# Kernel tuning notes

Hardware: AMD Instinct MI355X
Metric: run time of the kernel (lower is better)

## Reference

```python
import jax, jax.numpy as jnp
import numpy as np
from jax import lax

B, T, IN, H = 32, 512, 512, 512
NUM_LAYERS, NUM_DIR = 2, 2


def _lstm_layer(inputs, Wx, Wh, bx, bh, reverse):
    """inputs: [T,B,D]; Wx: [4H,D]; Wh: [4H,H]; bx,bh: [4H]. Returns (hs [T,B,H], hT, cT)."""
    Tn, Bn, _ = inputs.shape
    Hn = Wh.shape[1]
    # Precompute input-to-hidden projections for all timesteps (one big GEMM).
    xg = jnp.einsum('tbd,gd->tbg', inputs, Wx) + bx + bh  # [T,B,4H]
    if reverse:
        xg = xg[::-1]

    def step(carry, xg_t):
        h, c = carry
        g = xg_t + h @ Wh.T  # [B,4H]
        i, f, gg, o = jnp.split(g, 4, axis=-1)  # PyTorch LSTM gate order i,f,g,o
        i = jax.nn.sigmoid(i)
        f = jax.nn.sigmoid(f)
        gg = jnp.tanh(gg)
        o = jax.nn.sigmoid(o)
        c = f * c + i * gg
        h = o * jnp.tanh(c)
        return (h, c), h

    h0 = jnp.zeros((Bn, Hn), dtype=inputs.dtype)
    (hT, cT), hs = lax.scan(step, (h0, h0), xg)
    if reverse:
        hs = hs[::-1]
    return hs, hT, cT


def setup_inputs() -> dict:
    key = jax.random.key(0)
    ks = jax.random.split(key, 20)
    std = 1.0 / np.sqrt(H)
    u = lambda k, shp: jax.random.uniform(k, shp, jnp.float32, -std, std)
    inp = {
        'x': jax.random.normal(ks[0], (B, T, IN), jnp.float32),
        # layer 0: input dim IN, stacked over 2 directions
        'Wx_l0': u(ks[1], (NUM_DIR, 4 * H, IN)),
        'Wh_l0': u(ks[2], (NUM_DIR, 4 * H, H)),
        'bx_l0': u(ks[3], (NUM_DIR, 4 * H)),
        'bh_l0': u(ks[4], (NUM_DIR, 4 * H)),
        # layer 1: input dim 2H (bidirectional concat)
        'Wx_l1': u(ks[5], (NUM_DIR, 4 * H, NUM_DIR * H)),
        'Wh_l1': u(ks[6], (NUM_DIR, 4 * H, H)),
        'bx_l1': u(ks[7], (NUM_DIR, 4 * H)),
        'bh_l1': u(ks[8], (NUM_DIR, 4 * H)),
    }
    return inp


def reference(x, Wx_l0, Wh_l0, bx_l0, bh_l0, Wx_l1, Wh_l1, bx_l1, bh_l1):
    layer_params = [(Wx_l0, Wh_l0, bx_l0, bh_l0), (Wx_l1, Wh_l1, bx_l1, bh_l1)]
    inputs = jnp.transpose(x, (1, 0, 2))  # [T,B,IN] (batch_first -> time-major)
    h_list, c_list = [], []
    for layer in range(NUM_LAYERS):
        Wx, Wh, bx, bh = layer_params[layer]
        dir_outs = []
        for d in range(NUM_DIR):
            hs, hT, cT = _lstm_layer(inputs, Wx[d], Wh[d], bx[d], bh[d], reverse=(d == 1))
            dir_outs.append(hs)
            h_list.append(hT)
            c_list.append(cT)
        inputs = jnp.concatenate(dir_outs, axis=-1)  # [T,B,2H] (dropout=0.0)
    output = jnp.transpose(inputs, (1, 0, 2))  # [B,T,2H]
    h_n = jnp.stack(h_list)  # [num_layers*num_dir, B, H]
    c_n = jnp.stack(c_list)
    return output, h_n, c_n
```

## Files before the change

kernel.cpp:

```cpp
#include <hip/hip_runtime.h>

typedef _Float16 f16;
typedef _Float16 f16x2 __attribute__((ext_vector_type(2)));
typedef _Float16 f16x4 __attribute__((ext_vector_type(4)));
typedef _Float16 f16x8 __attribute__((ext_vector_type(8)));
typedef float f32x4 __attribute__((ext_vector_type(4)));

#define AS1 __attribute__((address_space(1)))
#define AS3 __attribute__((address_space(3)))

static __device__ __forceinline__ float sigf(float x) { return 1.f / (1.f + __expf(-x)); }
static __device__ __forceinline__ float tanh_f(float x) { return 2.f / (1.f + __expf(-2.f * x)) - 1.f; }

__global__ void f2h_kernel(const float* __restrict__ in, f16* __restrict__ out, int n4) {
  const int i = blockIdx.x * blockDim.x + threadIdx.x;
  if (i >= n4) return;
  const float4 v = ((const float4*)in)[i];
  f16x4 o;
  o[0] = (f16)v.x; o[1] = (f16)v.y; o[2] = (f16)v.z; o[3] = (f16)v.w;
  ((f16x4*)out)[i] = o;
}

__global__ void bias_kernel(const float* __restrict__ a, const float* __restrict__ b,
                            float* __restrict__ o, int n) {
  const int i = blockIdx.x * blockDim.x + threadIdx.x;
  if (i < n) o[i] = a[i] + b[i];
}

__global__ __launch_bounds__(256) void gemm_xg(const f16* __restrict__ A,
                                               const f16* __restrict__ Bt,
                                               const float* __restrict__ bias,
                                               f16* __restrict__ outp, int K) {
  __shared__ f16 As[128 * 64];
  __shared__ f16 Bs[128 * 64];
  const int tid = threadIdx.x;
  const int w = tid >> 6, l = tid & 63;
  const int m0 = blockIdx.x << 7, n0 = blockIdx.y << 7;
  const int wm = w >> 1, wn = w & 1;
  f32x4 acc[4][4] = {};

  const int lr8 = l >> 3, lc8 = l & 7;
  const int gcol = (lc8 ^ lr8) << 3;

  for (int k0 = 0; k0 < K; k0 += 64) {
    __syncthreads();
#pragma unroll
    for (int j = 0; j < 4; ++j) {
      const int i = (w << 2) + j;
      const f16* ga = A + (size_t)(m0 + (i << 3) + lr8) * K + (k0 + gcol);
      __builtin_amdgcn_global_load_lds((const AS1 void*)ga, (AS3 void*)(As + (i << 9)), 16, 0, 0);
      const f16* gb = Bt + (size_t)(n0 + (i << 3) + lr8) * K + (k0 + gcol);
      __builtin_amdgcn_global_load_lds((const AS1 void*)gb, (AS3 void*)(Bs + (i << 9)), 16, 0, 0);
    }
    asm volatile("s_waitcnt vmcnt(0)" ::: "memory");
    __syncthreads();

#pragma unroll
    for (int kk = 0; kk < 2; ++kk) {
      const int cb = (kk << 6) + ((l >> 4) << 4);
      f16x8 af[4], bf[4];
#pragma unroll
      for (int a = 0; a < 4; ++a) {
        const int r = (wm << 6) + (a << 4) + (l & 15);
        af[a] = *(const f16x8*)((const char*)As + r * 128 + (cb ^ ((r & 7) << 4)));
      }
#pragma unroll
      for (int b = 0; b < 4; ++b) {
        const int r = (wn << 6) + (b << 4) + (l & 15);
        bf[b] = *(const f16x8*)((const char*)Bs + r * 128 + (cb ^ ((r & 7) << 4)));
      }
#pragma unroll
      for (int a = 0; a < 4; ++a)
#pragma unroll
        for (int b = 0; b < 4; ++b)
          acc[a][b] = __builtin_amdgcn_mfma_f32_16x16x32_f16(af[a], bf[b], acc[a][b], 0, 0, 0);
    }
  }

#pragma unroll
  for (int b = 0; b < 4; ++b) {
    const int col = n0 + (wn << 6) + (b << 4) + (l & 15);
    const float bv = bias[col];
    f16* ob = outp + (size_t)(col >> 11) * (16384ull * 2048) + (col & 2047);
#pragma unroll
    for (int a = 0; a < 4; ++a) {
      const int row0 = m0 + (wm << 6) + (a << 4) + ((l >> 4) << 2);
#pragma unroll
      for (int r = 0; r < 4; ++r)
        ob[(size_t)(row0 + r) * 2048] = (f16)(acc[a][b][r] + bv);
    }
  }
}

__global__ __launch_bounds__(256) void lstm_scan(const f16* __restrict__ Whb,
                                                 const f16* __restrict__ xg,
                                                 unsigned long long* __restrict__ ring,
                                                 f16* __restrict__ h0_all,
                                                 float* __restrict__ outf,
                                                 float* __restrict__ hn,
                                                 float* __restrict__ cn,
                                                 const int layer) {
  __shared__ f16 Wh_s[64 * 512];
  __shared__ f16 h_s[32 * 512];
  __shared__ float G_s[4 * 32 * 18];

  const int tid = threadIdx.x;
  const int dir = blockIdx.x >> 5;
  const int s = blockIdx.x & 31;
  const int w = tid >> 6, l = tid & 63;

#pragma unroll
  for (int j = 0; j < 16; ++j) {
    const int chunk = (j << 8) + tid;
    const int lr = chunk >> 6;
    const int cbyte = (chunk & 63) << 4;
    const int g = lr >> 4, u = lr & 15;
    const char* src = (const char*)Whb + (((size_t)dir * 2048 + (g << 9) + (s << 4) + u) << 10) + cbyte;
    const uint4 v = *(const uint4*)src;
    *(uint4*)((char*)Wh_s + (lr << 10) + (cbyte ^ ((lr & 7) << 4))) = v;
  }

  unsigned long long* rdir = ring + ((size_t)dir << 15);
  const int bb = tid >> 3;
  const int up = tid & 7;

  float c0 = 0.f, c1 = 0.f;
  __syncthreads();

#pragma unroll 1
  for (int t = 0; t < 512; ++t) {
    const int tau = dir ? (511 - t) : t;
    const f16* xr = xg + (((size_t)dir * 16384 + (size_t)bb * 512 + (size_t)tau) << 11) + (s << 4) + (up << 1);
    const f16x2 xv0 = *(const f16x2*)(xr);
    const f16x2 xv1 = *(const f16x2*)(xr + 512);
    const f16x2 xv2 = *(const f16x2*)(xr + 1024);
    const f16x2 xv3 = *(const f16x2*)(xr + 1536);

    float pi0 = 0.f, pi1 = 0.f, pf0 = 0.f, pf1 = 0.f, pg0 = 0.f, pg1 = 0.f, po0 = 0.f, po1 = 0.f;

    if (t > 0) {
      const unsigned tgt = (unsigned)t;
      const unsigned long long* rs = rdir + ((size_t)(t & 3) << 13);
      unsigned long long v[8][4];
#pragma unroll
      for (int j = 0; j < 8; ++j) {
        const int chunk = (j << 8) + tid;
        const unsigned long long* sp = rs + ((chunk >> 6) << 8) + ((chunk & 63) << 2);
#pragma unroll
        for (int q = 0; q < 4; ++q)
          v[j][q] = __hip_atomic_load(sp + q, __ATOMIC_RELAXED, __HIP_MEMORY_SCOPE_AGENT);
      }
#pragma unroll
      for (int j = 0; j < 8; ++j) {
        const int chunk = (j << 8) + tid;
        const int b = chunk >> 6;
        const unsigned long long* sp = rs + (b << 8) + ((chunk & 63) << 2);
        int guard = 0;
        while (!(((unsigned)v[j][0] == tgt) & ((unsigned)v[j][1] == tgt) &
                 ((unsigned)v[j][2] == tgt) & ((unsigned)v[j][3] == tgt))) {
#pragma unroll
          for (int q = 0; q < 4; ++q)
            v[j][q] = __hip_atomic_load(sp + q, __ATOMIC_RELAXED, __HIP_MEMORY_SCOPE_AGENT);
          if (++guard > (1 << 20)) break;
        }
        uint4 d;
        d.x = (unsigned)(v[j][0] >> 32);
        d.y = (unsigned)(v[j][1] >> 32);
        d.z = (unsigned)(v[j][2] >> 32);
        d.w = (unsigned)(v[j][3] >> 32);
        const int cbyte = (chunk & 63) << 4;
        *(uint4*)((char*)h_s + (b << 10) + (cbyte ^ ((b & 7) << 4))) = d;
      }
      __syncthreads();

      f32x4 acc0 = {}, acc1 = {};
#pragma unroll
      for (int kk = 0; kk < 16; ++kk) {
        const int cb = (kk << 6) + ((l >> 4) << 4);
        const int ra0 = l & 15;
        const int ra1 = 16 + ra0;
        const int rb = (w << 4) + ra0;
        const f16x8 a0 = *(const f16x8*)((const char*)h_s + (ra0 << 10) + (cb ^ ((ra0 & 7) << 4)));
        const f16x8 a1 = *(const f16x8*)((const char*)h_s + (ra1 << 10) + (cb ^ ((ra1 & 7) << 4)));
        const f16x8 bv = *(const f16x8*)((const char*)Wh_s + (rb << 10) + (cb ^ ((rb & 7) << 4)));
        acc0 = __builtin_amdgcn_mfma_f32_16x16x32_f16(a0, bv, acc0, 0, 0, 0);
        acc1 = __builtin_amdgcn_mfma_f32_16x16x32_f16(a1, bv, acc1, 0, 0, 0);
      }
#pragma unroll
      for (int r = 0; r < 4; ++r) {
        const int dr = ((l >> 4) << 2) + r;
        G_s[((w << 5) + dr) * 18 + (l & 15)] = acc0[r];
        G_s[((w << 5) + 16 + dr) * 18 + (l & 15)] = acc1[r];
      }
      __syncthreads();

      const float* gp = G_s + bb * 18 + (up << 1);
      const float2 vi = *(const float2*)(gp);
      const float2 vf = *(const float2*)(gp + 576);
      const float2 vg = *(const float2*)(gp + 1152);
      const float2 vo = *(const float2*)(gp + 1728);
      pi0 = vi.x; pi1 = vi.y; pf0 = vf.x; pf1 = vf.y;
      pg0 = vg.x; pg1 = vg.y; po0 = vo.x; po1 = vo.y;
    }

    pi0 += (float)xv0[0]; pi1 += (float)xv0[1];
    pf0 += (float)xv1[0]; pf1 += (float)xv1[1];
    pg0 += (float)xv2[0]; pg1 += (float)xv2[1];
    po0 += (float)xv3[0]; po1 += (float)xv3[1];

    const float i0 = sigf(pi0), i1 = sigf(pi1);
    const float f0 = sigf(pf0), f1 = sigf(pf1);
    const float g0 = tanh_f(pg0), g1 = tanh_f(pg1);
    const float o0 = sigf(po0), o1 = sigf(po1);
    c0 = f0 * c0 + i0 * g0;
    c1 = f1 * c1 + i1 * g1;
    const float h0v = o0 * tanh_f(c0);
    const float h1v = o1 * tanh_f(c1);

    union { f16x2 h2; unsigned u; } pk;
    pk.h2[0] = (f16)h0v; pk.h2[1] = (f16)h1v;

    {
      const size_t ridx = ((size_t)((t + 1) & 3) << 13) + ((size_t)bb << 8) + (s << 3) + up;
      const unsigned long long pv = ((unsigned long long)pk.u << 32) | (unsigned long long)(t + 1);
      __hip_atomic_store(rdir + ridx, pv, __ATOMIC_RELAXED, __HIP_MEMORY_SCOPE_AGENT);
    }

    const size_t orow = (((size_t)bb * 512 + (size_t)tau) << 10) + ((size_t)dir << 9) + (s << 4) + (up << 1);
    if (layer == 0) {
      *(unsigned*)(h0_all + orow) = pk.u;
    } else {
      *(float2*)(outf + orow) = make_float2(h0v, h1v);
    }
    if (t == 511) {
      const size_t nidx = (((size_t)(layer << 1) + (size_t)dir) << 14) + ((size_t)bb << 9) + (s << 4) + (up << 1);
      *(float2*)(hn + nidx) = make_float2(h0v, h1v);
      *(float2*)(cn + nidx) = make_float2(c0, c1);
    }
  }
}

extern "C" void kernel_launch(void* const* d_in, const int* in_sizes, int n_in,
                              void* d_out, int out_size, void* d_ws, size_t ws_size,
                              hipStream_t stream) {
  const float* x = (const float*)d_in[0];
  const float* Wx0 = (const float*)d_in[1];
  const float* Wh0 = (const float*)d_in[2];
  const float* bx0 = (const float*)d_in[3];
  const float* bh0 = (const float*)d_in[4];
  const float* Wx1 = (const float*)d_in[5];
  const float* Wh1 = (const float*)d_in[6];
  const float* bx1 = (const float*)d_in[7];
  const float* bh1 = (const float*)d_in[8];

  char* ws = (char*)d_ws;
  size_t off = 0;
  auto alloc = [&](size_t b) { char* p = ws + off; off += (b + 255) & ~(size_t)255; return p; };
  f16* xg = (f16*)alloc(2ull * 16384 * 2048 * 2);
  f16* x_h = (f16*)alloc(16384ull * 512 * 2);
  f16* h0a = (f16*)alloc(16384ull * 1024 * 2);
  f16* Wx0h = (f16*)alloc(2ull * 2048 * 512 * 2);
  f16* Wh0h = (f16*)alloc(2ull * 2048 * 512 * 2);
  f16* Wx1h = (f16*)alloc(2ull * 2048 * 1024 * 2);
  f16* Wh1h = (f16*)alloc(2ull * 2048 * 512 * 2);
  float* bias0 = (float*)alloc(4096 * 4);
  float* bias1 = (float*)alloc(4096 * 4);
  unsigned long long* ring0 = (unsigned long long*)alloc(2ull * 4 * 32 * 256 * 8);
  unsigned long long* ring1 = (unsigned long long*)alloc(2ull * 4 * 32 * 256 * 8);
  if (off > ws_size) return;

  float* outp = (float*)d_out;
  float* hn = outp + 16384ull * 1024;
  float* cn = hn + 4ull * 32 * 512;

  hipMemsetAsync(ring0, 0, 2ull * 4 * 32 * 256 * 8, stream);
  hipMemsetAsync(ring1, 0, 2ull * 4 * 32 * 256 * 8, stream);

  f2h_kernel<<<dim3(2097152 / 256), 256, 0, stream>>>(x, x_h, 2097152);
  f2h_kernel<<<dim3(524288 / 256), 256, 0, stream>>>(Wx0, Wx0h, 524288);
  f2h_kernel<<<dim3(524288 / 256), 256, 0, stream>>>(Wh0, Wh0h, 524288);
  f2h_kernel<<<dim3(1048576 / 256), 256, 0, stream>>>(Wx1, Wx1h, 1048576);
  f2h_kernel<<<dim3(524288 / 256), 256, 0, stream>>>(Wh1, Wh1h, 524288);
  bias_kernel<<<16, 256, 0, stream>>>(bx0, bh0, bias0, 4096);
  bias_kernel<<<16, 256, 0, stream>>>(bx1, bh1, bias1, 4096);

  dim3 g(128, 32);
  gemm_xg<<<g, 256, 0, stream>>>(x_h, Wx0h, bias0, xg, 512);
  lstm_scan<<<64, 256, 0, stream>>>(Wh0h, xg, ring0, h0a, nullptr, hn, cn, 0);
  gemm_xg<<<g, 256, 0, stream>>>(h0a, Wx1h, bias1, xg, 1024);
  lstm_scan<<<64, 256, 0, stream>>>(Wh1h, xg, ring1, nullptr, outp, hn, cn, 1);
}
```

Measured before the change: 5.187 ms.

## Add per-block step counters for polling and batch output stores over eight steps

Each block now publishes its completed step in a small per-direction counter array. Waiting blocks first spin on these 32 counters and only then read the h ring once, instead of spinning on every ring entry. The ring tag becomes step XOR payload, so a stale value cannot pass the check. Output h stores are buffered in registers for eight timesteps and written together, which moves global writes off the serial recurrence path. The costs are an extra barrier per step and a counter store that, being relaxed with no fence, could become visible before the ring data, which the retained per-entry check still covers.

```diff
diff --git a/kernel.cpp b/kernel.cpp
--- a/kernel.cpp
+++ b/kernel.cpp
@@ -95,6 +95,7 @@
 __global__ __launch_bounds__(256) void lstm_scan(const f16* __restrict__ Whb,
                                                  const f16* __restrict__ xg,
                                                  unsigned long long* __restrict__ ring,
+                                                 unsigned* __restrict__ sums,
                                                  f16* __restrict__ h0_all,
                                                  float* __restrict__ outf,
                                                  float* __restrict__ hn,
@@ -121,121 +122,150 @@
   }
 
   unsigned long long* rdir = ring + ((size_t)dir << 15);
+  unsigned* sum = sums + (((layer << 1) + dir) << 6);
   const int bb = tid >> 3;
   const int up = tid & 7;
 
   float c0 = 0.f, c1 = 0.f;
   __syncthreads();
 
-#pragma unroll 1
-  for (int t = 0; t < 512; ++t) {
-    const int tau = dir ? (511 - t) : t;
-    const f16* xr = xg + (((size_t)dir * 16384 + (size_t)bb * 512 + (size_t)tau) << 11) + (s << 4) + (up << 1);
-    const f16x2 xv0 = *(const f16x2*)(xr);
-    const f16x2 xv1 = *(const f16x2*)(xr + 512);
-    const f16x2 xv2 = *(const f16x2*)(xr + 1024);
-    const f16x2 xv3 = *(const f16x2*)(xr + 1536);
-
-    float pi0 = 0.f, pi1 = 0.f, pf0 = 0.f, pf1 = 0.f, pg0 = 0.f, pg1 = 0.f, po0 = 0.f, po1 = 0.f;
-
-    if (t > 0) {
-      const unsigned tgt = (unsigned)t;
-      const unsigned long long* rs = rdir + ((size_t)(t & 3) << 13);
-      unsigned long long v[8][4];
-#pragma unroll
-      for (int j = 0; j < 8; ++j) {
-        const int chunk = (j << 8) + tid;
-        const unsigned long long* sp = rs + ((chunk >> 6) << 8) + ((chunk & 63) << 2);
-#pragma unroll
-        for (int q = 0; q < 4; ++q)
-          v[j][q] = __hip_atomic_load(sp + q, __ATOMIC_RELAXED, __HIP_MEMORY_SCOPE_AGENT);
-      }
-#pragma unroll
-      for (int j = 0; j < 8; ++j) {
-        const int chunk = (j << 8) + tid;
-        const int b = chunk >> 6;
-        const unsigned long long* sp = rs + (b << 8) + ((chunk & 63) << 2);
-        int guard = 0;
-        while (!(((unsigned)v[j][0] == tgt) & ((unsigned)v[j][1] == tgt) &
-                 ((unsigned)v[j][2] == tgt) & ((unsigned)v[j][3] == tgt))) {
+  for (int tb = 0; tb < 512; tb += 8) {
+    unsigned svh[8];
+    float2 svo[8];
+#pragma unroll
+    for (int ti = 0; ti < 8; ++ti) {
+      const int t = tb + ti;
+      const int tau = dir ? (511 - t) : t;
+      float pi0 = 0.f, pi1 = 0.f, pf0 = 0.f, pf1 = 0.f, pg0 = 0.f, pg1 = 0.f, po0 = 0.f, po1 = 0.f;
+
+      if (t > 0) {
+        const unsigned tgt = (unsigned)t;
+        {
+          const unsigned* sw = sum + (tid & 31);
+          int guard = 0;
+          unsigned v;
+          do {
+            v = __hip_atomic_load(sw, __ATOMIC_RELAXED, __HIP_MEMORY_SCOPE_AGENT);
+          } while (v < tgt && ++guard < (1 << 20));
+        }
+        __syncthreads();
+
+        const unsigned long long* rs = rdir + ((size_t)(t & 3) << 13);
+        unsigned long long v[8][4];
+#pragma unroll
+        for (int j = 0; j < 8; ++j) {
+          const int chunk = (j << 8) + tid;
+          const unsigned long long* sp = rs + ((chunk >> 6) << 8) + ((chunk & 63) << 2);
 #pragma unroll
           for (int q = 0; q < 4; ++q)
             v[j][q] = __hip_atomic_load(sp + q, __ATOMIC_RELAXED, __HIP_MEMORY_SCOPE_AGENT);
-          if (++guard > (1 << 20)) break;
-        }
-        uint4 d;
-        d.x = (unsigned)(v[j][0] >> 32);
-        d.y = (unsigned)(v[j][1] >> 32);
-        d.z = (unsigned)(v[j][2] >> 32);
-        d.w = (unsigned)(v[j][3] >> 32);
-        const int cbyte = (chunk & 63) << 4;
-        *(uint4*)((char*)h_s + (b << 10) + (cbyte ^ ((b & 7) << 4))) = d;
-      }
-      __syncthreads();
-
-      f32x4 acc0 = {}, acc1 = {};
-#pragma unroll
-      for (int kk = 0; kk < 16; ++kk) {
-        const int cb = (kk << 6) + ((l >> 4) << 4);
-        const int ra0 = l & 15;
-        const int ra1 = 16 + ra0;
-        const int rb = (w << 4) + ra0;
-        const f16x8 a0 = *(const f16x8*)((const char*)h_s + (ra0 << 10) + (cb ^ ((ra0 & 7) << 4)));
-        const f16x8 a1 = *(const f16x8*)((const char*)h_s + (ra1 << 10) + (cb ^ ((ra1 & 7) << 4)));
-        const f16x8 bv = *(const f16x8*)((const char*)Wh_s + (rb << 10) + (cb ^ ((rb & 7) << 4)));
-        acc0 = __builtin_amdgcn_mfma_f32_16x16x32_f16(a0, bv, acc0, 0, 0, 0);
-        acc1 = __builtin_amdgcn_mfma_f32_16x16x32_f16(a1, bv, acc1, 0, 0, 0);
-      }
-#pragma unroll
-      for (int r = 0; r < 4; ++r) {
-        const int dr = ((l >> 4) << 2) + r;
-        G_s[((w << 5) + dr) * 18 + (l & 15)] = acc0[r];
-        G_s[((w << 5) + 16 + dr) * 18 + (l & 15)] = acc1[r];
-      }
-      __syncthreads();
-
-      const float* gp = G_s + bb * 18 + (up << 1);
-      const float2 vi = *(const float2*)(gp);
-      const float2 vf = *(const float2*)(gp + 576);
-      const float2 vg = *(const float2*)(gp + 1152);
-      const float2 vo = *(const float2*)(gp + 1728);
-      pi0 = vi.x; pi1 = vi.y; pf0 = vf.x; pf1 = vf.y;
-      pg0 = vg.x; pg1 = vg.y; po0 = vo.x; po1 = vo.y;
-    }
-
-    pi0 += (float)xv0[0]; pi1 += (float)xv0[1];
-    pf0 += (float)xv1[0]; pf1 += (float)xv1[1];
-    pg0 += (float)xv2[0]; pg1 += (float)xv2[1];
-    po0 += (float)xv3[0]; po1 += (float)xv3[1];
-
-    const float i0 = sigf(pi0), i1 = sigf(pi1);
-    const float f0 = sigf(pf0), f1 = sigf(pf1);
-    const float g0 = tanh_f(pg0), g1 = tanh_f(pg1);
-    const float o0 = sigf(po0), o1 = sigf(po1);
-    c0 = f0 * c0 + i0 * g0;
-    c1 = f1 * c1 + i1 * g1;
-    const float h0v = o0 * tanh_f(c0);
-    const float h1v = o1 * tanh_f(c1);
-
-    union { f16x2 h2; unsigned u; } pk;
-    pk.h2[0] = (f16)h0v; pk.h2[1] = (f16)h1v;
-
-    {
-      const size_t ridx = ((size_t)((t + 1) & 3) << 13) + ((size_t)bb << 8) + (s << 3) + up;
-      const unsigned long long pv = ((unsigned long long)pk.u << 32) | (unsigned long long)(t + 1);
-      __hip_atomic_store(rdir + ridx, pv, __ATOMIC_RELAXED, __HIP_MEMORY_SCOPE_AGENT);
-    }
-
-    const size_t orow = (((size_t)bb * 512 + (size_t)tau) << 10) + ((size_t)dir << 9) + (s << 4) + (up << 1);
-    if (layer == 0) {
-      *(unsigned*)(h0_all + orow) = pk.u;
-    } else {
-      *(float2*)(outf + orow) = make_float2(h0v, h1v);
-    }
-    if (t == 511) {
-      const size_t nidx = (((size_t)(layer << 1) + (size_t)dir) << 14) + ((size_t)bb << 9) + (s << 4) + (up << 1);
-      *(float2*)(hn + nidx) = make_float2(h0v, h1v);
-      *(float2*)(cn + nidx) = make_float2(c0, c1);
+        }
+#pragma unroll
+        for (int j = 0; j < 8; ++j) {
+          const int chunk = (j << 8) + tid;
+          const int b = chunk >> 6;
+          const unsigned long long* sp = rs + (b << 8) + ((chunk & 63) << 2);
+          int guard = 0;
+          while (!((((unsigned)v[j][0] ^ (unsigned)(v[j][0] >> 32)) == tgt) &
+                   (((unsigned)v[j][1] ^ (unsigned)(v[j][1] >> 32)) == tgt) &
+                   (((unsigned)v[j][2] ^ (unsigned)(v[j][2] >> 32)) == tgt) &
+                   (((unsigned)v[j][3] ^ (unsigned)(v[j][3] >> 32)) == tgt))) {
+#pragma unroll
+            for (int q = 0; q < 4; ++q)
+              v[j][q] = __hip_atomic_load(sp + q, __ATOMIC_RELAXED, __HIP_MEMORY_SCOPE_AGENT);
+            if (++guard > (1 << 20)) break;
+          }
+          uint4 d;
+          d.x = (unsigned)(v[j][0] >> 32);
+          d.y = (unsigned)(v[j][1] >> 32);
+          d.z = (unsigned)(v[j][2] >> 32);
+          d.w = (unsigned)(v[j][3] >> 32);
+          const int cbyte = (chunk & 63) << 4;
+          *(uint4*)((char*)h_s + (b << 10) + (cbyte ^ ((b & 7) << 4))) = d;
+        }
+        __syncthreads();
+      }
+
+      const f16* xr = xg + (((size_t)dir * 16384 + (size_t)bb * 512 + (size_t)tau) << 11) + (s << 4) + (up << 1);
+      const f16x2 xv0 = *(const f16x2*)(xr);
+      const f16x2 xv1 = *(const f16x2*)(xr + 512);
+      const f16x2 xv2 = *(const f16x2*)(xr + 1024);
+      const f16x2 xv3 = *(const f16x2*)(xr + 1536);
+
+      if (t > 0) {
+        f32x4 acc0 = {}, acc1 = {};
+#pragma unroll
+        for (int kk = 0; kk < 16; ++kk) {
+          const int cb = (kk << 6) + ((l >> 4) << 4);
+          const int ra0 = l & 15;
+          const int ra1 = 16 + ra0;
+          const int rb = (w << 4) + ra0;
+          const f16x8 a0 = *(const f16x8*)((const char*)h_s + (ra0 << 10) + (cb ^ ((ra0 & 7) << 4)));
+          const f16x8 a1 = *(const f16x8*)((const char*)h_s + (ra1 << 10) + (cb ^ ((ra1 & 7) << 4)));
+          const f16x8 bv = *(const f16x8*)((const char*)Wh_s + (rb << 10) + (cb ^ ((rb & 7) << 4)));
+          acc0 = __builtin_amdgcn_mfma_f32_16x16x32_f16(a0, bv, acc0, 0, 0, 0);
+          acc1 = __builtin_amdgcn_mfma_f32_16x16x32_f16(a1, bv, acc1, 0, 0, 0);
+        }
+#pragma unroll
+        for (int r = 0; r < 4; ++r) {
+          const int dr = ((l >> 4) << 2) + r;
+          G_s[((w << 5) + dr) * 18 + (l & 15)] = acc0[r];
+          G_s[((w << 5) + 16 + dr) * 18 + (l & 15)] = acc1[r];
+        }
+        __syncthreads();
+
+        const float* gp = G_s + bb * 18 + (up << 1);
+        const float2 vi = *(const float2*)(gp);
+        const float2 vf = *(const float2*)(gp + 576);
+        const float2 vg = *(const float2*)(gp + 1152);
+        const float2 vo = *(const float2*)(gp + 1728);
+        pi0 = vi.x; pi1 = vi.y; pf0 = vf.x; pf1 = vf.y;
+        pg0 = vg.x; pg1 = vg.y; po0 = vo.x; po1 = vo.y;
+      }
+
+      pi0 += (float)xv0[0]; pi1 += (float)xv0[1];
+      pf0 += (float)xv1[0]; pf1 += (float)xv1[1];
+      pg0 += (float)xv2[0]; pg1 += (float)xv2[1];
+      po0 += (float)xv3[0]; po1 += (float)xv3[1];
+
+      const float i0 = sigf(pi0), i1 = sigf(pi1);
+      const float f0 = sigf(pf0), f1 = sigf(pf1);
+      const float g0 = tanh_f(pg0), g1 = tanh_f(pg1);
+      const float o0 = sigf(po0), o1 = sigf(po1);
+      c0 = f0 * c0 + i0 * g0;
+      c1 = f1 * c1 + i1 * g1;
+      const float h0v = o0 * tanh_f(c0);
+      const float h1v = o1 * tanh_f(c1);
+
+      union { f16x2 h2; unsigned u; } pk;
+      pk.h2[0] = (f16)h0v; pk.h2[1] = (f16)h1v;
+
+      {
+        const size_t ridx = ((size_t)((t + 1) & 3) << 13) + ((size_t)bb << 8) + (s << 3) + up;
+        const unsigned long long pv =
+            ((unsigned long long)pk.u << 32) | (unsigned long long)((unsigned)(t + 1) ^ pk.u);
+        __hip_atomic_store(rdir + ridx, pv, __ATOMIC_RELAXED, __HIP_MEMORY_SCOPE_AGENT);
+      }
+      if (tid == 0)
+        __hip_atomic_store(sum + s, (unsigned)(t + 1), __ATOMIC_RELAXED, __HIP_MEMORY_SCOPE_AGENT);
+
+      if (layer == 0) svh[ti] = pk.u;
+      else            svo[ti] = make_float2(h0v, h1v);
+
+      if (t == 511) {
+        const size_t nidx = (((size_t)(layer << 1) + (size_t)dir) << 14) + ((size_t)bb << 9) + (s << 4) + (up << 1);
+        *(float2*)(hn + nidx) = make_float2(h0v, h1v);
+        *(float2*)(cn + nidx) = make_float2(c0, c1);
+      }
+    }
+
+#pragma unroll
+    for (int ti = 0; ti < 8; ++ti) {
+      const int t = tb + ti;
+      const int tau = dir ? (511 - t) : t;
+      const size_t orow = (((size_t)bb * 512 + (size_t)tau) << 10) + ((size_t)dir << 9) + (s << 4) + (up << 1);
+      if (layer == 0) *(unsigned*)(h0_all + orow) = svh[ti];
+      else            *(float2*)(outf + orow) = svo[ti];
     }
   }
 }
@@ -267,6 +297,7 @@
   float* bias1 = (float*)alloc(4096 * 4);
   unsigned long long* ring0 = (unsigned long long*)alloc(2ull * 4 * 32 * 256 * 8);
   unsigned long long* ring1 = (unsigned long long*)alloc(2ull * 4 * 32 * 256 * 8);
+  unsigned* sums = (unsigned*)alloc(4ull * 64 * 4);
   if (off > ws_size) return;
 
   float* outp = (float*)d_out;
@@ -275,6 +306,7 @@
 
   hipMemsetAsync(ring0, 0, 2ull * 4 * 32 * 256 * 8, stream);
   hipMemsetAsync(ring1, 0, 2ull * 4 * 32 * 256 * 8, stream);
+  hipMemsetAsync(sums, 0, 4ull * 64 * 4, stream);
 
   f2h_kernel<<<dim3(2097152 / 256), 256, 0, stream>>>(x, x_h, 2097152);
   f2h_kernel<<<dim3(524288 / 256), 256, 0, stream>>>(Wx0, Wx0h, 524288);
@@ -286,7 +318,7 @@
 
   dim3 g(128, 32);
   gemm_xg<<<g, 256, 0, stream>>>(x_h, Wx0h, bias0, xg, 512);
-  lstm_scan<<<64, 256, 0, stream>>>(Wh0h, xg, ring0, h0a, nullptr, hn, cn, 0);
+  lstm_scan<<<64, 256, 0, stream>>>(Wh0h, xg, ring0, sums, h0a, nullptr, hn, cn, 0);
   gemm_xg<<<g, 256, 0, stream>>>(h0a, Wx1h, bias1, xg, 1024);
-  lstm_scan<<<64, 256, 0, stream>>>(Wh1h, xg, ring1, nullptr, outp, hn, cn, 1);
-}
+  lstm_scan<<<64, 256, 0, stream>>>(Wh1h, xg, ring1, sums, nullptr, outp, hn, cn, 1);
+}
```

Result: slower. 6.604 ms (+27.3%).

## Process both directions per block with 8 hidden units each in LSTM scan

Applied to the files above, without the earlier changes.

Each scan block now handles 8 hidden units for both directions instead of 16 units for one direction. The grid size is not visible in this excerpt, but it is presumably still 64 blocks. The two directions are interleaved within each timestep, so one direction's ring polling can overlap with the other's work, and the per-direction MFMA tile shrinks to 32x32. Each thread now computes a single hidden unit, with lane shuffles packing pairs for the ring and output stores. The two ring memsets are merged into one, which assumes the two allocations are contiguous. The cost is two ring waits and four syncthreads per step, serialized inside one block.

```diff
diff --git a/kernel.cpp b/kernel.cpp
--- a/kernel.cpp
+++ b/kernel.cpp
@@ -100,142 +100,131 @@
                                                  float* __restrict__ hn,
                                                  float* __restrict__ cn,
                                                  const int layer) {
-  __shared__ f16 Wh_s[64 * 512];
+  __shared__ f16 Wh_s[2 * 32 * 512];
   __shared__ f16 h_s[32 * 512];
-  __shared__ float G_s[4 * 32 * 18];
+  __shared__ float G_s[32 * 36];
 
   const int tid = threadIdx.x;
-  const int dir = blockIdx.x >> 5;
-  const int s = blockIdx.x & 31;
-  const int w = tid >> 6, l = tid & 63;
+  const int s6 = blockIdx.x;
+  const int l = tid & 63;
+  const int w = tid >> 6;
+  const int wm = w >> 1, wn = w & 1;
 
 #pragma unroll
   for (int j = 0; j < 16; ++j) {
-    const int chunk = (j << 8) + tid;
-    const int lr = chunk >> 6;
-    const int cbyte = (chunk & 63) << 4;
-    const int g = lr >> 4, u = lr & 15;
-    const char* src = (const char*)Whb + (((size_t)dir * 2048 + (g << 9) + (s << 4) + u) << 10) + cbyte;
+    const int c = (j << 8) + tid;
+    const int d = c >> 11;
+    const int lr = (c >> 6) & 31;
+    const int cb = (c & 63) << 4;
+    const int g = lr >> 3, u = lr & 7;
+    const char* src = (const char*)Whb + (((size_t)d * 2048 + (g << 9) + (s6 << 3) + u) << 10) + cb;
     const uint4 v = *(const uint4*)src;
-    *(uint4*)((char*)Wh_s + (lr << 10) + (cbyte ^ ((lr & 7) << 4))) = v;
-  }
-
-  unsigned long long* rdir = ring + ((size_t)dir << 15);
+    *(uint4*)((char*)Wh_s + (d << 15) + (lr << 10) + (cb ^ ((lr & 7) << 4))) = v;
+  }
+
   const int bb = tid >> 3;
-  const int up = tid & 7;
-
-  float c0 = 0.f, c1 = 0.f;
+  const int uu = tid & 7;
+  float cst0 = 0.f, cst1 = 0.f;
   __syncthreads();
 
 #pragma unroll 1
   for (int t = 0; t < 512; ++t) {
-    const int tau = dir ? (511 - t) : t;
-    const f16* xr = xg + (((size_t)dir * 16384 + (size_t)bb * 512 + (size_t)tau) << 11) + (s << 4) + (up << 1);
-    const f16x2 xv0 = *(const f16x2*)(xr);
-    const f16x2 xv1 = *(const f16x2*)(xr + 512);
-    const f16x2 xv2 = *(const f16x2*)(xr + 1024);
-    const f16x2 xv3 = *(const f16x2*)(xr + 1536);
-
-    float pi0 = 0.f, pi1 = 0.f, pf0 = 0.f, pf1 = 0.f, pg0 = 0.f, pg1 = 0.f, po0 = 0.f, po1 = 0.f;
-
-    if (t > 0) {
-      const unsigned tgt = (unsigned)t;
-      const unsigned long long* rs = rdir + ((size_t)(t & 3) << 13);
-      unsigned long long v[8][4];
-#pragma unroll
-      for (int j = 0; j < 8; ++j) {
-        const int chunk = (j << 8) + tid;
-        const unsigned long long* sp = rs + ((chunk >> 6) << 8) + ((chunk & 63) << 2);
-#pragma unroll
-        for (int q = 0; q < 4; ++q)
-          v[j][q] = __hip_atomic_load(sp + q, __ATOMIC_RELAXED, __HIP_MEMORY_SCOPE_AGENT);
-      }
-#pragma unroll
-      for (int j = 0; j < 8; ++j) {
-        const int chunk = (j << 8) + tid;
-        const int b = chunk >> 6;
-        const unsigned long long* sp = rs + (b << 8) + ((chunk & 63) << 2);
-        int guard = 0;
-        while (!(((unsigned)v[j][0] == tgt) & ((unsigned)v[j][1] == tgt) &
-                 ((unsigned)v[j][2] == tgt) & ((unsigned)v[j][3] == tgt))) {
+#pragma unroll
+    for (int d = 0; d < 2; ++d) {
+      const int tau = d ? (511 - t) : t;
+      const f16* xr = xg + (((size_t)d * 16384 + (size_t)bb * 512 + (size_t)tau) << 11) + (s6 << 3) + uu;
+      float pi = (float)xr[0];
+      float pf = (float)xr[512];
+      float pg = (float)xr[1024];
+      float po = (float)xr[1536];
+      unsigned long long* rdir = ring + ((size_t)d << 15);
+
+      if (t > 0) {
+        const unsigned tgt = (unsigned)t;
+        const unsigned long long* rs = rdir + ((size_t)(t & 3) << 13);
+        unsigned long long v[8][4];
+#pragma unroll
+        for (int j = 0; j < 8; ++j) {
+          const int c = (j << 8) + tid;
+          const unsigned long long* sp = rs + ((c >> 6) << 8) + ((c & 63) << 2);
 #pragma unroll
           for (int q = 0; q < 4; ++q)
             v[j][q] = __hip_atomic_load(sp + q, __ATOMIC_RELAXED, __HIP_MEMORY_SCOPE_AGENT);
-          if (++guard > (1 << 20)) break;
         }
-        uint4 d;
-        d.x = (unsigned)(v[j][0] >> 32);
-        d.y = (unsigned)(v[j][1] >> 32);
-        d.z = (unsigned)(v[j][2] >> 32);
-        d.w = (unsigned)(v[j][3] >> 32);
-        const int cbyte = (chunk & 63) << 4;
-        *(uint4*)((char*)h_s + (b << 10) + (cbyte ^ ((b & 7) << 4))) = d;
-      }
-      __syncthreads();
-
-      f32x4 acc0 = {}, acc1 = {};
-#pragma unroll
-      for (int kk = 0; kk < 16; ++kk) {
-        const int cb = (kk << 6) + ((l >> 4) << 4);
-        const int ra0 = l & 15;
-        const int ra1 = 16 + ra0;
-        const int rb = (w << 4) + ra0;
-        const f16x8 a0 = *(const f16x8*)((const char*)h_s + (ra0 << 10) + (cb ^ ((ra0 & 7) << 4)));
-        const f16x8 a1 = *(const f16x8*)((const char*)h_s + (ra1 << 10) + (cb ^ ((ra1 & 7) << 4)));
-        const f16x8 bv = *(const f16x8*)((const char*)Wh_s + (rb << 10) + (cb ^ ((rb & 7) << 4)));
-        acc0 = __builtin_amdgcn_mfma_f32_16x16x32_f16(a0, bv, acc0, 0, 0, 0);
-        acc1 = __builtin_amdgcn_mfma_f32_16x16x32_f16(a1, bv, acc1, 0, 0, 0);
-      }
-#pragma unroll
-      for (int r = 0; r < 4; ++r) {
-        const int dr = ((l >> 4) << 2) + r;
-        G_s[((w << 5) + dr) * 18 + (l & 15)] = acc0[r];
-        G_s[((w << 5) + 16 + dr) * 18 + (l & 15)] = acc1[r];
-      }
-      __syncthreads();
-
-      const float* gp = G_s + bb * 18 + (up << 1);
-      const float2 vi = *(const float2*)(gp);
-      const float2 vf = *(const float2*)(gp + 576);
-      const float2 vg = *(const float2*)(gp + 1152);
-      const float2 vo = *(const float2*)(gp + 1728);
-      pi0 = vi.x; pi1 = vi.y; pf0 = vf.x; pf1 = vf.y;
-      pg0 = vg.x; pg1 = vg.y; po0 = vo.x; po1 = vo.y;
-    }
-
-    pi0 += (float)xv0[0]; pi1 += (float)xv0[1];
-    pf0 += (float)xv1[0]; pf1 += (float)xv1[1];
-    pg0 += (float)xv2[0]; pg1 += (float)xv2[1];
-    po0 += (float)xv3[0]; po1 += (float)xv3[1];
-
-    const float i0 = sigf(pi0), i1 = sigf(pi1);
-    const float f0 = sigf(pf0), f1 = sigf(pf1);
-    const float g0 = tanh_f(pg0), g1 = tanh_f(pg1);
-    const float o0 = sigf(po0), o1 = sigf(po1);
-    c0 = f0 * c0 + i0 * g0;
-    c1 = f1 * c1 + i1 * g1;
-    const float h0v = o0 * tanh_f(c0);
-    const float h1v = o1 * tanh_f(c1);
-
-    union { f16x2 h2; unsigned u; } pk;
-    pk.h2[0] = (f16)h0v; pk.h2[1] = (f16)h1v;
-
-    {
-      const size_t ridx = ((size_t)((t + 1) & 3) << 13) + ((size_t)bb << 8) + (s << 3) + up;
-      const unsigned long long pv = ((unsigned long long)pk.u << 32) | (unsigned long long)(t + 1);
-      __hip_atomic_store(rdir + ridx, pv, __ATOMIC_RELAXED, __HIP_MEMORY_SCOPE_AGENT);
-    }
-
-    const size_t orow = (((size_t)bb * 512 + (size_t)tau) << 10) + ((size_t)dir << 9) + (s << 4) + (up << 1);
-    if (layer == 0) {
-      *(unsigned*)(h0_all + orow) = pk.u;
-    } else {
-      *(float2*)(outf + orow) = make_float2(h0v, h1v);
-    }
-    if (t == 511) {
-      const size_t nidx = (((size_t)(layer << 1) + (size_t)dir) << 14) + ((size_t)bb << 9) + (s << 4) + (up << 1);
-      *(float2*)(hn + nidx) = make_float2(h0v, h1v);
-      *(float2*)(cn + nidx) = make_float2(c0, c1);
+#pragma unroll
+        for (int j = 0; j < 8; ++j) {
+          const int c = (j << 8) + tid;
+          const int b = c >> 6;
+          const unsigned long long* sp = rs + (b << 8) + ((c & 63) << 2);
+          int guard = 0;
+          while (!(((unsigned)v[j][0] == tgt) & ((unsigned)v[j][1] == tgt) &
+                   ((unsigned)v[j][2] == tgt) & ((unsigned)v[j][3] == tgt))) {
+#pragma unroll
+            for (int q = 0; q < 4; ++q)
+              v[j][q] = __hip_atomic_load(sp + q, __ATOMIC_RELAXED, __HIP_MEMORY_SCOPE_AGENT);
+            if (++guard > (1 << 20)) break;
+          }
+          uint4 dd;
+          dd.x = (unsigned)(v[j][0] >> 32);
+          dd.y = (unsigned)(v[j][1] >> 32);
+          dd.z = (unsigned)(v[j][2] >> 32);
+          dd.w = (unsigned)(v[j][3] >> 32);
+          const int cb = (c & 63) << 4;
+          *(uint4*)((char*)h_s + (b << 10) + (cb ^ ((b & 7) << 4))) = dd;
+        }
+        __syncthreads();
+
+        f32x4 acc = {};
+#pragma unroll
+        for (int kk = 0; kk < 16; ++kk) {
+          const int cb = (kk << 6) + ((l >> 4) << 4);
+          const int ra = (wm << 4) + (l & 15);
+          const int rb = (wn << 4) + (l & 15);
+          const f16x8 av = *(const f16x8*)((const char*)h_s + (ra << 10) + (cb ^ ((ra & 7) << 4)));
+          const f16x8 bv = *(const f16x8*)((const char*)Wh_s + (d << 15) + (rb << 10) + (cb ^ ((rb & 7) << 4)));
+          acc = __builtin_amdgcn_mfma_f32_16x16x32_f16(av, bv, acc, 0, 0, 0);
+        }
+#pragma unroll
+        for (int r = 0; r < 4; ++r)
+          G_s[((wm << 4) + ((l >> 4) << 2) + r) * 36 + (wn << 4) + (l & 15)] = acc[r];
+        __syncthreads();
+
+        const float* gp = G_s + bb * 36 + uu;
+        pi += gp[0];
+        pf += gp[8];
+        pg += gp[16];
+        po += gp[24];
+      }
+
+      const float iv = sigf(pi), fv = sigf(pf), gv = tanh_f(pg), ov = sigf(po);
+      float& cs = d ? cst1 : cst0;
+      cs = fv * cs + iv * gv;
+      const float hv = ov * tanh_f(cs);
+
+      union { f16 h; unsigned short us; } hb;
+      hb.h = (f16)hv;
+      const unsigned mine = hb.us;
+      const unsigned other = (unsigned)__shfl_xor((int)mine, 1);
+      const unsigned pk = (other << 16) | mine;
+      const float hod = __shfl_xor(hv, 1);
+
+      if (!(uu & 1)) {
+        const size_t ridx = ((size_t)((t + 1) & 3) << 13) + ((size_t)bb << 8) + (s6 << 2) + (uu >> 1);
+        const unsigned long long pv = ((unsigned long long)pk << 32) | (unsigned long long)(t + 1);
+        __hip_atomic_store(rdir + ridx, pv, __ATOMIC_RELAXED, __HIP_MEMORY_SCOPE_AGENT);
+      }
+
+      const size_t orow = (((size_t)bb * 512 + (size_t)tau) << 10) + ((size_t)d << 9) + (s6 << 3) + uu;
+      if (layer == 0) {
+        if (!(uu & 1)) *(unsigned*)(h0_all + orow) = pk;
+      } else {
+        if (!(uu & 1)) *(float2*)(outf + orow) = make_float2(hv, hod);
+      }
+      if (t == 511) {
+        const size_t nidx = (((size_t)(layer << 1) + (size_t)d) << 14) + (size_t)bb * 512 + (s6 << 3) + uu;
+        hn[nidx] = hv;
+        cn[nidx] = cs;
+      }
     }
   }
 }
@@ -265,16 +254,16 @@
   f16* Wh1h = (f16*)alloc(2ull * 2048 * 512 * 2);
   float* bias0 = (float*)alloc(4096 * 4);
   float* bias1 = (float*)alloc(4096 * 4);
-  unsigned long long* ring0 = (unsigned long long*)alloc(2ull * 4 * 32 * 256 * 8);
-  unsigned long long* ring1 = (unsigned long long*)alloc(2ull * 4 * 32 * 256 * 8);
+  const size_t RB = 2ull * 4 * 32 * 256 * 8;
+  unsigned long long* ring0 = (unsigned long long*)alloc(RB);
+  unsigned long long* ring1 = (unsigned long long*)alloc(RB);
   if (off > ws_size) return;
 
   float* outp = (float*)d_out;
   float* hn = outp + 16384ull * 1024;
   float* cn = hn + 4ull * 32 * 512;
 
-  hipMemsetAsync(ring0, 0, 2ull * 4 * 32 * 256 * 8, stream);
-  hipMemsetAsync(ring1, 0, 2ull * 4 * 32 * 256 * 8, stream);
+  hipMemsetAsync(ring0, 0, 2 * RB, stream);
 
   f2h_kernel<<<dim3(2097152 / 256), 256, 0, stream>>>(x, x_h, 2097152);
   f2h_kernel<<<dim3(524288 / 256), 256, 0, stream>>>(Wx0, Wx0h, 524288);
```

After: 8.481 ms. +63.5%, slower.

## Remap LSTM scan so each wave owns its gates, cutting a barrier per step

Applied to the files above, without the earlier changes.

Reorders the Wh rows assigned to each wave so that one wave's MFMA output holds all four gates for its own hidden units. The gate exchange then runs through a per-wave shared buffer guarded by an LDS wait instead of a block-wide barrier. It also double-buffers h_s so the next step's writes cannot overwrite data still being read, and prefetches the next timestep's xg values one iteration ahead. The two ring memsets are merged into one call. This removes one __syncthreads and hides the xg load latency on the serial recurrence path, but depends on the lane-to-unit remapping and the wave-local LDS ordering being correct.

```diff
diff --git a/kernel.cpp b/kernel.cpp
--- a/kernel.cpp
+++ b/kernel.cpp
@@ -101,8 +101,8 @@
                                                  float* __restrict__ cn,
                                                  const int layer) {
   __shared__ f16 Wh_s[64 * 512];
-  __shared__ f16 h_s[32 * 512];
-  __shared__ float G_s[4 * 32 * 18];
+  __shared__ f16 h_s[2][32 * 512];
+  __shared__ float G_s[4][32 * 20];
 
   const int tid = threadIdx.x;
   const int dir = blockIdx.x >> 5;
@@ -121,21 +121,23 @@
   }
 
   unsigned long long* rdir = ring + ((size_t)dir << 15);
-  const int bb = tid >> 3;
-  const int up = tid & 7;
+  const int b32 = l & 31;
+  const int vp = l >> 5;
+  const int ug = (s << 4) + (w << 2) + (vp << 1);
+  float* Gw = (float*)&G_s[w][0];
 
   float c0 = 0.f, c1 = 0.f;
   __syncthreads();
+
+  const f16* xr0 = xg + (((size_t)dir * 16384 + (size_t)b32 * 512 + (dir ? 511 : 0)) << 11) + ug;
+  f16x2 xc0 = *(const f16x2*)(xr0);
+  f16x2 xc1 = *(const f16x2*)(xr0 + 512);
+  f16x2 xc2 = *(const f16x2*)(xr0 + 1024);
+  f16x2 xc3 = *(const f16x2*)(xr0 + 1536);
 
 #pragma unroll 1
   for (int t = 0; t < 512; ++t) {
     const int tau = dir ? (511 - t) : t;
-    const f16* xr = xg + (((size_t)dir * 16384 + (size_t)bb * 512 + (size_t)tau) << 11) + (s << 4) + (up << 1);
-    const f16x2 xv0 = *(const f16x2*)(xr);
-    const f16x2 xv1 = *(const f16x2*)(xr + 512);
-    const f16x2 xv2 = *(const f16x2*)(xr + 1024);
-    const f16x2 xv3 = *(const f16x2*)(xr + 1536);
-
     float pi0 = 0.f, pi1 = 0.f, pf0 = 0.f, pf1 = 0.f, pg0 = 0.f, pg1 = 0.f, po0 = 0.f, po1 = 0.f;
 
     if (t > 0) {
@@ -150,6 +152,7 @@
         for (int q = 0; q < 4; ++q)
           v[j][q] = __hip_atomic_load(sp + q, __ATOMIC_RELAXED, __HIP_MEMORY_SCOPE_AGENT);
       }
+      char* hb = (char*)&h_s[t & 1][0];
 #pragma unroll
       for (int j = 0; j < 8; ++j) {
         const int chunk = (j << 8) + tid;
@@ -169,44 +172,62 @@
         d.z = (unsigned)(v[j][2] >> 32);
         d.w = (unsigned)(v[j][3] >> 32);
         const int cbyte = (chunk & 63) << 4;
-        *(uint4*)((char*)h_s + (b << 10) + (cbyte ^ ((b & 7) << 4))) = d;
+        *(uint4*)(hb + (b << 10) + (cbyte ^ ((b & 7) << 4))) = d;
       }
       __syncthreads();
-
+    }
+
+    f16x2 xn0, xn1, xn2, xn3;
+    {
+      const int t2 = (t < 511) ? (t + 1) : t;
+      const int tau2 = dir ? (511 - t2) : t2;
+      const f16* xr = xg + (((size_t)dir * 16384 + (size_t)b32 * 512 + tau2) << 11) + ug;
+      xn0 = *(const f16x2*)(xr);
+      xn1 = *(const f16x2*)(xr + 512);
+      xn2 = *(const f16x2*)(xr + 1024);
+      xn3 = *(const f16x2*)(xr + 1536);
+    }
+
+    if (t > 0) {
+      const char* hb = (const char*)&h_s[t & 1][0];
       f32x4 acc0 = {}, acc1 = {};
 #pragma unroll
       for (int kk = 0; kk < 16; ++kk) {
         const int cb = (kk << 6) + ((l >> 4) << 4);
-        const int ra0 = l & 15;
-        const int ra1 = 16 + ra0;
-        const int rb = (w << 4) + ra0;
-        const f16x8 a0 = *(const f16x8*)((const char*)h_s + (ra0 << 10) + (cb ^ ((ra0 & 7) << 4)));
-        const f16x8 a1 = *(const f16x8*)((const char*)h_s + (ra1 << 10) + (cb ^ ((ra1 & 7) << 4)));
+        const int n = l & 15;
+        const int ra0 = n;
+        const int ra1 = 16 + n;
+        const int rb = ((n >> 2) << 4) + (w << 2) + (n & 3);
+        const f16x8 a0 = *(const f16x8*)(hb + (ra0 << 10) + (cb ^ ((ra0 & 7) << 4)));
+        const f16x8 a1 = *(const f16x8*)(hb + (ra1 << 10) + (cb ^ ((ra1 & 7) << 4)));
         const f16x8 bv = *(const f16x8*)((const char*)Wh_s + (rb << 10) + (cb ^ ((rb & 7) << 4)));
         acc0 = __builtin_amdgcn_mfma_f32_16x16x32_f16(a0, bv, acc0, 0, 0, 0);
         acc1 = __builtin_amdgcn_mfma_f32_16x16x32_f16(a1, bv, acc1, 0, 0, 0);
       }
-#pragma unroll
-      for (int r = 0; r < 4; ++r) {
-        const int dr = ((l >> 4) << 2) + r;
-        G_s[((w << 5) + dr) * 18 + (l & 15)] = acc0[r];
-        G_s[((w << 5) + 16 + dr) * 18 + (l & 15)] = acc1[r];
-      }
-      __syncthreads();
-
-      const float* gp = G_s + bb * 18 + (up << 1);
-      const float2 vi = *(const float2*)(gp);
-      const float2 vf = *(const float2*)(gp + 576);
-      const float2 vg = *(const float2*)(gp + 1152);
-      const float2 vo = *(const float2*)(gp + 1728);
-      pi0 = vi.x; pi1 = vi.y; pf0 = vf.x; pf1 = vf.y;
-      pg0 = vg.x; pg1 = vg.y; po0 = vo.x; po1 = vo.y;
-    }
-
-    pi0 += (float)xv0[0]; pi1 += (float)xv0[1];
-    pf0 += (float)xv1[0]; pf1 += (float)xv1[1];
-    pg0 += (float)xv2[0]; pg1 += (float)xv2[1];
-    po0 += (float)xv3[0]; po1 += (float)xv3[1];
+      {
+        const int n = l & 15;
+        const int c = ((n & 3) << 2) + (n >> 2);
+#pragma unroll
+        for (int r = 0; r < 4; ++r) {
+          const int br = ((l >> 4) << 2) + r;
+          Gw[br * 20 + c] = acc0[r];
+          Gw[(16 + br) * 20 + c] = acc1[r];
+        }
+      }
+      asm volatile("s_waitcnt lgkmcnt(0)" ::: "memory");
+      __builtin_amdgcn_sched_barrier(0);
+      {
+        const float4 ga = *(const float4*)(Gw + b32 * 20 + (vp << 3));
+        const float4 gb = *(const float4*)(Gw + b32 * 20 + (vp << 3) + 4);
+        pi0 = ga.x; pf0 = ga.y; pg0 = ga.z; po0 = ga.w;
+        pi1 = gb.x; pf1 = gb.y; pg1 = gb.z; po1 = gb.w;
+      }
+    }
+
+    pi0 += (float)xc0[0]; pi1 += (float)xc0[1];
+    pf0 += (float)xc1[0]; pf1 += (float)xc1[1];
+    pg0 += (float)xc2[0]; pg1 += (float)xc2[1];
+    po0 += (float)xc3[0]; po1 += (float)xc3[1];
 
     const float i0 = sigf(pi0), i1 = sigf(pi1);
     const float f0 = sigf(pf0), f1 = sigf(pf1);
@@ -221,22 +242,24 @@
     pk.h2[0] = (f16)h0v; pk.h2[1] = (f16)h1v;
 
     {
-      const size_t ridx = ((size_t)((t + 1) & 3) << 13) + ((size_t)bb << 8) + (s << 3) + up;
+      const size_t ridx = ((size_t)((t + 1) & 3) << 13) + ((size_t)b32 << 8) + (ug >> 1);
       const unsigned long long pv = ((unsigned long long)pk.u << 32) | (unsigned long long)(t + 1);
       __hip_atomic_store(rdir + ridx, pv, __ATOMIC_RELAXED, __HIP_MEMORY_SCOPE_AGENT);
     }
 
-    const size_t orow = (((size_t)bb * 512 + (size_t)tau) << 10) + ((size_t)dir << 9) + (s << 4) + (up << 1);
+    const size_t orow = (((size_t)b32 * 512 + (size_t)tau) << 10) + ((size_t)dir << 9) + ug;
     if (layer == 0) {
       *(unsigned*)(h0_all + orow) = pk.u;
     } else {
       *(float2*)(outf + orow) = make_float2(h0v, h1v);
     }
     if (t == 511) {
-      const size_t nidx = (((size_t)(layer << 1) + (size_t)dir) << 14) + ((size_t)bb << 9) + (s << 4) + (up << 1);
+      const size_t nidx = (((size_t)(layer << 1) + (size_t)dir) << 14) + ((size_t)b32 << 9) + ug;
       *(float2*)(hn + nidx) = make_float2(h0v, h1v);
       *(float2*)(cn + nidx) = make_float2(c0, c1);
     }
+
+    xc0 = xn0; xc1 = xn1; xc2 = xn2; xc3 = xn3;
   }
 }
 
@@ -265,16 +288,16 @@
   f16* Wh1h = (f16*)alloc(2ull * 2048 * 512 * 2);
   float* bias0 = (float*)alloc(4096 * 4);
   float* bias1 = (float*)alloc(4096 * 4);
-  unsigned long long* ring0 = (unsigned long long*)alloc(2ull * 4 * 32 * 256 * 8);
-  unsigned long long* ring1 = (unsigned long long*)alloc(2ull * 4 * 32 * 256 * 8);
+  const size_t RB = 2ull * 4 * 32 * 256 * 8;
+  unsigned long long* ring0 = (unsigned long long*)alloc(RB);
+  unsigned long long* ring1 = (unsigned long long*)alloc(RB);
   if (off > ws_size) return;
 
   float* outp = (float*)d_out;
   float* hn = outp + 16384ull * 1024;
   float* cn = hn + 4ull * 32 * 512;
 
-  hipMemsetAsync(ring0, 0, 2ull * 4 * 32 * 256 * 8, stream);
-  hipMemsetAsync(ring1, 0, 2ull * 4 * 32 * 256 * 8, stream);
+  hipMemsetAsync(ring0, 0, 2 * RB, stream);
 
   f2h_kernel<<<dim3(2097152 / 256), 256, 0, stream>>>(x, x_h, 2097152);
   f2h_kernel<<<dim3(524288 / 256), 256, 0, stream>>>(Wx0, Wx0h, 524288);
```

Result: slower. 5.698 ms (+9.8%).
